# Kernel optimization log

Measured on AMD Instinct MI355X. Metric: run time of the kernel, lower is better.

## Reference

```python
import jax, jax.numpy as jnp
import numpy as np

T, B, D_IN, H = 512, 128, 1024, 2048

def _lstm_cell(x, h, c, W_ih, W_hh, b):
    # PyTorch LSTMCell gate order: i, f, g, o
    gates = x @ W_ih.T + h @ W_hh.T + b  # [B, 4H]
    i, f, g, o = jnp.split(gates, 4, axis=-1)
    c_new = jax.nn.sigmoid(f) * c + jax.nn.sigmoid(i) * jnp.tanh(g)
    h_new = jax.nn.sigmoid(o) * jnp.tanh(c_new)
    return h_new, c_new

def setup_inputs() -> dict:
    key = jax.random.key(0)
    ks = jax.random.split(key, 12)
    k = 1.0 / np.sqrt(H)  # torch LSTMCell init range
    u = lambda kk, shape: jax.random.uniform(kk, shape, jnp.float32, -k, k)
    return {
        "input_seq": jax.random.normal(ks[0], (T, B, D_IN), jnp.float32),
        "h0": jax.random.normal(ks[1], (2, B, H), jnp.float32),
        "c0": jax.random.normal(ks[2], (2, B, H), jnp.float32),
        "W_ih0": u(ks[3], (4 * H, D_IN)),
        "W_hh0": u(ks[4], (4 * H, H)),
        "b0": u(ks[5], (4 * H,)),
        "W_ih1": u(ks[6], (4 * H, H)),
        "W_hh1": u(ks[7], (4 * H, H)),
        "b1": u(ks[8], (4 * H,)),
    }

def reference(input_seq, h0, c0, W_ih0, W_hh0, b0, W_ih1, W_hh1, b1):
    def step(carry, x_t):
        h0_, c0_, h1_, c1_ = carry
        h0n, c0n = _lstm_cell(x_t, h0_, c0_, W_ih0, W_hh0, b0)
        h1n, c1n = _lstm_cell(h0n, h1_, c1_, W_ih1, W_hh1, b1)
        return (h0n, c0n, h1n, c1n), None

    init = (h0[0], c0[0], h0[1], c0[1])
    (h0f, c0f, h1f, c1f), _ = jax.lax.scan(step, init, input_seq)
    return h1f  # last layer hidden at final timestep [B, H]
```

## Files before the change

### kernel.cpp

```cpp
#include <hip/hip_runtime.h>
#include <stdint.h>
#include <stddef.h>

#define T_STEPS 512
#define B_SZ    128
#define DIN     1024
#define H_SZ    2048
#define NG      8192
#define BH      (B_SZ * H_SZ)

typedef __attribute__((ext_vector_type(8))) short bf16x8;
typedef __attribute__((ext_vector_type(4))) float f32x4;

static __device__ __forceinline__ unsigned short f2bf(float x) {
  unsigned int u = __float_as_uint(x);
  u += 0x7fffu + ((u >> 16) & 1u);
  return (unsigned short)(u >> 16);
}

static __device__ __forceinline__ float sigm(float x) {
  return 1.0f / (1.0f + __expf(-x));
}
static __device__ __forceinline__ float tanh_(float x) {
  float e = __expf(-2.0f * fabsf(x));
  float t = (1.0f - e) / (1.0f + e);
  return x < 0.0f ? -t : t;
}

static __device__ __forceinline__ void async_load16(const void* gsrc, void* ldst) {
  __builtin_amdgcn_global_load_lds(
      (__attribute__((address_space(1))) void*)(const_cast<void*>(gsrc)),
      (__attribute__((address_space(3))) void*)ldst,
      16, 0, 0);
}

static __device__ __forceinline__ void wg_barrier_pinned() {
  __builtin_amdgcn_s_barrier();
  asm volatile("" ::: "memory");
  __builtin_amdgcn_sched_barrier(0);
}

__global__ void cvt_x_bf16(const float4* __restrict__ in, ushort4* __restrict__ out, int n4) {
  int i = blockIdx.x * blockDim.x + threadIdx.x;
  int st = gridDim.x * blockDim.x;
  for (; i < n4; i += st) {
    float4 v = in[i];
    ushort4 o;
    o.x = f2bf(v.x); o.y = f2bf(v.y); o.z = f2bf(v.z); o.w = f2bf(v.w);
    out[i] = o;
  }
}

__global__ void build_wcat(const float* __restrict__ wa, const float* __restrict__ wb,
                           unsigned short* __restrict__ outw, int ka, int K) {
  int k = blockIdx.x * blockDim.x + threadIdx.x;
  int n = blockIdx.y;
  if (k >= K) return;
  int kb = K - ka;
  float v = (k < ka) ? wa[(size_t)n * ka + k]
                     : wb[(size_t)n * kb + (k - ka)];
  outw[(size_t)n * K + k] = f2bf(v);
}

__global__ void init_state(const float* __restrict__ h0, const float* __restrict__ c0,
                           unsigned short* __restrict__ hb0, unsigned short* __restrict__ hb1,
                           float* __restrict__ cws) {
  int i = blockIdx.x * blockDim.x + threadIdx.x;
  if (i < BH) {
    hb0[i] = f2bf(h0[i]);
    hb1[i] = f2bf(h0[BH + i]);
    cws[i] = c0[i];
    cws[BH + i] = c0[BH + i];
  }
}

template<int K, int KSPLIT>
static __device__ __forceinline__ void lstm_step_body(
    unsigned short (*Bbuf)[128 * 64],
    const unsigned short* __restrict__ a0,
    const unsigned short* __restrict__ a1,
    const unsigned short* __restrict__ w,
    const float* __restrict__ bias,
    float* __restrict__ c,
    unsigned short* __restrict__ hout,
    float* __restrict__ fout,
    int tid, int lane, int wv, int n0h)
{
  constexpr int KT = K >> 6;
  f32x4 acc[8] = {};

  const int arow = wv * 16 + (lane & 15);
  const unsigned short* r0p = a0 + (size_t)arow * KSPLIT;
  const unsigned short* r1p = a1 + (size_t)arow * H_SZ;
  const int klo = (lane >> 4) << 3;

  auto loadA = [&](int kt, bf16x8 (&A)[2]) {
    const int kb = kt << 6;
    const bool sA = kb < KSPLIT;
    const unsigned short* bp = (sA ? r0p : r1p) + (sA ? kb : kb - KSPLIT) + klo;
    A[0] = *(const bf16x8*)(bp);
    A[1] = *(const bf16x8*)(bp + 32);
  };

  auto stageB = [&](int kt) {
    const int kb = kt << 6;
#pragma unroll
    for (int it = 0; it < 2; ++it) {
      int cid = it * 512 + tid;
      int nl  = cid >> 3;
      int chs = (cid & 7) ^ (nl & 7);
      int nn  = ((nl >> 5) << 11) + n0h + (nl & 31);
      const unsigned short* src = w + (size_t)nn * K + kb + (chs << 3);
      async_load16(src, &Bbuf[kt & 3][(it * 512 + wv * 64) * 8]);
    }
  };

  auto iter = [&](int kt, bf16x8 (&A)[2]) {
    if (kt + 3 < KT) stageB(kt + 3);
    const int bq = kt & 3;
#pragma unroll
    for (int kkk = 0; kkk < 2; ++kkk) {
      const int ch = kkk * 4 + (lane >> 4);
      const int cswz = (ch ^ (lane & 7)) << 3;
      bf16x8 bfr[8];
#pragma unroll
      for (int ct = 0; ct < 8; ++ct)
        bfr[ct] = *(const bf16x8*)&Bbuf[bq][(ct * 16 + (lane & 15)) * 64 + cswz];
#pragma unroll
      for (int ct = 0; ct < 8; ++ct)
        acc[ct] = __builtin_amdgcn_mfma_f32_16x16x32_bf16(A[kkk], bfr[ct], acc[ct], 0, 0, 0);
    }
    if (kt + 4 < KT) loadA(kt + 4, A);
    int rem = KT - 1 - kt;
    if (rem >= 4)      asm volatile("s_waitcnt vmcnt(10)" ::: "memory");
    else if (rem == 3) asm volatile("s_waitcnt vmcnt(8)"  ::: "memory");
    else if (rem == 2) asm volatile("s_waitcnt vmcnt(4)"  ::: "memory");
    else if (rem == 1) asm volatile("s_waitcnt vmcnt(0)"  ::: "memory");
    wg_barrier_pinned();
  };

  asm volatile("s_waitcnt vmcnt(0)" ::: "memory");

  bf16x8 A0[2], A1[2], A2[2], A3[2];
  stageB(0); loadA(0, A0);
  stageB(1); loadA(1, A1);
  stageB(2); loadA(2, A2);
  loadA(3, A3);
  asm volatile("s_waitcnt vmcnt(12)" ::: "memory");
  wg_barrier_pinned();

  for (int kt = 0; kt < KT; kt += 4) {
    iter(kt,     A0);
    iter(kt + 1, A1);
    iter(kt + 2, A2);
    iter(kt + 3, A3);
  }

#pragma unroll
  for (int p = 0; p < 2; ++p) {
    const int hc = n0h + p * 16 + (lane & 15);
    const float bi  = bias[hc];
    const float bff = bias[H_SZ + hc];
    const float bg  = bias[2 * H_SZ + hc];
    const float bo  = bias[3 * H_SZ + hc];
#pragma unroll
    for (int r = 0; r < 4; ++r) {
      int row = wv * 16 + ((lane >> 4) << 2) + r;
      size_t idx = (size_t)row * H_SZ + hc;
      float iv = sigm(acc[p    ][r] + bi);
      float fv = sigm(acc[p + 2][r] + bff);
      float gv = tanh_(acc[p + 4][r] + bg);
      float ov = sigm(acc[p + 6][r] + bo);
      float cn = fv * c[idx] + iv * gv;
      c[idx] = cn;
      float hn = ov * tanh_(cn);
      hout[idx] = f2bf(hn);
      if (fout) fout[idx] = hn;
    }
  }
}

template<int K, int KSPLIT>
__global__ __launch_bounds__(512, 2) void lstm_one(
    const unsigned short* __restrict__ a0, const unsigned short* __restrict__ a1,
    const unsigned short* __restrict__ w,  const float* __restrict__ bias,
    float* __restrict__ c, unsigned short* __restrict__ hout, float* __restrict__ fout)
{
  __shared__ __align__(16) unsigned short Bbuf[4][128 * 64];
  const int tid = threadIdx.x, lane = tid & 63, wv = tid >> 6;
  const int n0h = blockIdx.x << 5;
  lstm_step_body<K, KSPLIT>(Bbuf, a0, a1, w, bias, c, hout, fout, tid, lane, wv, n0h);
}

template<int K1, int KS1, int K2, int KS2>
__global__ __launch_bounds__(512, 2) void lstm_pair(
    const unsigned short* __restrict__ a0_1, const unsigned short* __restrict__ a1_1,
    const unsigned short* __restrict__ w1,   const float* __restrict__ bias1,
    float* __restrict__ c1, unsigned short* __restrict__ h1out,
    const unsigned short* __restrict__ a0_2, const unsigned short* __restrict__ a1_2,
    const unsigned short* __restrict__ w2,   const float* __restrict__ bias2,
    float* __restrict__ c2, unsigned short* __restrict__ h2out)
{
  __shared__ __align__(16) unsigned short Bbuf[4][128 * 64];
  const int tid = threadIdx.x, lane = tid & 63, wv = tid >> 6;
  if (blockIdx.x < 64) {
    const int n0h = blockIdx.x << 5;
    lstm_step_body<K1, KS1>(Bbuf, a0_1, a1_1, w1, bias1, c1, h1out, nullptr, tid, lane, wv, n0h);
  } else {
    const int n0h = (blockIdx.x - 64) << 5;
    lstm_step_body<K2, KS2>(Bbuf, a0_2, a1_2, w2, bias2, c2, h2out, nullptr, tid, lane, wv, n0h);
  }
}

extern "C" void kernel_launch(void* const* d_in, const int* in_sizes, int n_in,
                              void* d_out, int out_size, void* d_ws, size_t ws_size,
                              hipStream_t stream) {
  (void)in_sizes; (void)n_in; (void)out_size; (void)ws_size;
  const float* x    = (const float*)d_in[0];
  const float* h0   = (const float*)d_in[1];
  const float* c0   = (const float*)d_in[2];
  const float* Wih0 = (const float*)d_in[3];
  const float* Whh0 = (const float*)d_in[4];
  const float* b0   = (const float*)d_in[5];
  const float* Wih1 = (const float*)d_in[6];
  const float* Whh1 = (const float*)d_in[7];
  const float* b1   = (const float*)d_in[8];
  float* out = (float*)d_out;

  unsigned short* xbf = (unsigned short*)d_ws;
  unsigned short* Wc0 = xbf + (size_t)T_STEPS * B_SZ * DIN;
  unsigned short* Wc1 = Wc0 + (size_t)NG * 3072;
  unsigned short* hb0 = Wc1 + (size_t)NG * 4096;
  unsigned short* hb1 = hb0 + 2 * (size_t)BH;
  float*          cws = (float*)(hb1 + 2 * (size_t)BH);

  cvt_x_bf16<<<dim3(4096), dim3(256), 0, stream>>>(
      (const float4*)x, (ushort4*)xbf, T_STEPS * B_SZ * DIN / 4);
  build_wcat<<<dim3(12, NG), dim3(256), 0, stream>>>(Wih0, Whh0, Wc0, DIN, 3072);
  build_wcat<<<dim3(16, NG), dim3(256), 0, stream>>>(Wih1, Whh1, Wc1, H_SZ, 4096);
  init_state<<<dim3(BH / 256), dim3(256), 0, stream>>>(h0, c0, hb0, hb1, cws);

  lstm_one<3072, 1024><<<dim3(64), dim3(512), 0, stream>>>(
      xbf, hb0 + 0, Wc0, b0, cws, hb0 + BH, nullptr);

  for (int t = 0; t < T_STEPS - 1; ++t) {
    const unsigned short* h0cur = hb0 + (size_t)((t + 1) & 1) * BH;
    lstm_pair<4096, 2048, 3072, 1024><<<dim3(128), dim3(512), 0, stream>>>(
           h0cur, hb1 + (size_t)(t & 1) * BH, Wc1, b1,
                    cws + BH, hb1 + (size_t)((t + 1) & 1) * BH,
         xbf + (size_t)(t + 1) * B_SZ * DIN, h0cur, Wc0, b0,
                    cws, hb0 + (size_t)(t & 1) * BH);
  }
  lstm_one<4096, 2048><<<dim3(64), dim3(512), 0, stream>>>(
      hb0 + 0, hb1 + BH, Wc1, b1, cws + BH, hb1 + 0, out);
}
```

Measured before the change: 23.29 ms.

## Switch LSTM step GEMM to 32x32x16 MFMA with 4-wave workgroups

Replaces the 16x16x32 bf16 MFMA tiling with 32x32x16 tiles. Each wave now covers 32 batch rows and all 128 gate columns using four 16-wide accumulators. Workgroups shrink from 512 to 256 threads (4 waves), so each thread stages four LDS chunks per k-tile, and the vmcnt thresholds and epilogue row mapping are updated to match. The larger MFMA shape reduces LDS B-fragment reads per FLOP, and the barrier after the last k-tile is skipped. The cost is fewer waves per workgroup for hiding latency and more accumulator registers per thread.

Measured after the change: 26.35 ms. 13.1% more time.

```diff
diff --git a/kernel.cpp b/kernel.cpp
--- a/kernel.cpp
+++ b/kernel.cpp
@@ -10,7 +10,7 @@
 #define BH      (B_SZ * H_SZ)
 
 typedef __attribute__((ext_vector_type(8))) short bf16x8;
-typedef __attribute__((ext_vector_type(4))) float f32x4;
+typedef __attribute__((ext_vector_type(16))) float f32x16;
 
 static __device__ __forceinline__ unsigned short f2bf(float x) {
   unsigned int u = __float_as_uint(x);
@@ -87,66 +87,66 @@
     int tid, int lane, int wv, int n0h)
 {
   constexpr int KT = K >> 6;
-  f32x4 acc[8] = {};
-
-  const int arow = wv * 16 + (lane & 15);
+  f32x16 acc[4] = {};
+
+  const int arow = wv * 32 + (lane & 31);
   const unsigned short* r0p = a0 + (size_t)arow * KSPLIT;
   const unsigned short* r1p = a1 + (size_t)arow * H_SZ;
-  const int klo = (lane >> 4) << 3;
-
-  auto loadA = [&](int kt, bf16x8 (&A)[2]) {
+  const int khi = (lane >> 5) << 3;
+
+  auto loadA = [&](int kt, bf16x8 (&A)[4]) {
     const int kb = kt << 6;
     const bool sA = kb < KSPLIT;
-    const unsigned short* bp = (sA ? r0p : r1p) + (sA ? kb : kb - KSPLIT) + klo;
-    A[0] = *(const bf16x8*)(bp);
-    A[1] = *(const bf16x8*)(bp + 32);
+    const unsigned short* bp = (sA ? r0p : r1p) + (sA ? kb : kb - KSPLIT) + khi;
+#pragma unroll
+    for (int cc = 0; cc < 4; ++cc)
+      A[cc] = *(const bf16x8*)(bp + cc * 16);
   };
 
   auto stageB = [&](int kt) {
     const int kb = kt << 6;
 #pragma unroll
-    for (int it = 0; it < 2; ++it) {
-      int cid = it * 512 + tid;
+    for (int it = 0; it < 4; ++it) {
+      int cid = it * 256 + tid;
       int nl  = cid >> 3;
       int chs = (cid & 7) ^ (nl & 7);
       int nn  = ((nl >> 5) << 11) + n0h + (nl & 31);
       const unsigned short* src = w + (size_t)nn * K + kb + (chs << 3);
-      async_load16(src, &Bbuf[kt & 3][(it * 512 + wv * 64) * 8]);
+      async_load16(src, &Bbuf[kt & 3][(it * 256 + wv * 64) * 8]);
     }
   };
 
-  auto iter = [&](int kt, bf16x8 (&A)[2]) {
+  auto iter = [&](int kt, bf16x8 (&A)[4]) {
     if (kt + 3 < KT) stageB(kt + 3);
     const int bq = kt & 3;
 #pragma unroll
-    for (int kkk = 0; kkk < 2; ++kkk) {
-      const int ch = kkk * 4 + (lane >> 4);
-      const int cswz = (ch ^ (lane & 7)) << 3;
-      bf16x8 bfr[8];
-#pragma unroll
-      for (int ct = 0; ct < 8; ++ct)
-        bfr[ct] = *(const bf16x8*)&Bbuf[bq][(ct * 16 + (lane & 15)) * 64 + cswz];
-#pragma unroll
-      for (int ct = 0; ct < 8; ++ct)
-        acc[ct] = __builtin_amdgcn_mfma_f32_16x16x32_bf16(A[kkk], bfr[ct], acc[ct], 0, 0, 0);
+    for (int cc = 0; cc < 4; ++cc) {
+      const int chunk = (((cc << 1) + (lane >> 5)) ^ (lane & 7)) << 3;
+      bf16x8 bfr[4];
+#pragma unroll
+      for (int ct = 0; ct < 4; ++ct)
+        bfr[ct] = *(const bf16x8*)&Bbuf[bq][(ct * 32 + (lane & 31)) * 64 + chunk];
+#pragma unroll
+      for (int ct = 0; ct < 4; ++ct)
+        acc[ct] = __builtin_amdgcn_mfma_f32_32x32x16_bf16(A[cc], bfr[ct], acc[ct], 0, 0, 0);
     }
     if (kt + 4 < KT) loadA(kt + 4, A);
     int rem = KT - 1 - kt;
-    if (rem >= 4)      asm volatile("s_waitcnt vmcnt(10)" ::: "memory");
-    else if (rem == 3) asm volatile("s_waitcnt vmcnt(8)"  ::: "memory");
-    else if (rem == 2) asm volatile("s_waitcnt vmcnt(4)"  ::: "memory");
+    if (rem >= 4)      asm volatile("s_waitcnt vmcnt(20)" ::: "memory");
+    else if (rem == 3) asm volatile("s_waitcnt vmcnt(16)" ::: "memory");
+    else if (rem == 2) asm volatile("s_waitcnt vmcnt(8)"  ::: "memory");
     else if (rem == 1) asm volatile("s_waitcnt vmcnt(0)"  ::: "memory");
-    wg_barrier_pinned();
+    if (rem > 0) wg_barrier_pinned();
   };
 
   asm volatile("s_waitcnt vmcnt(0)" ::: "memory");
 
-  bf16x8 A0[2], A1[2], A2[2], A3[2];
+  bf16x8 A0[4], A1[4], A2[4], A3[4];
   stageB(0); loadA(0, A0);
   stageB(1); loadA(1, A1);
   stageB(2); loadA(2, A2);
   loadA(3, A3);
-  asm volatile("s_waitcnt vmcnt(12)" ::: "memory");
+  asm volatile("s_waitcnt vmcnt(24)" ::: "memory");
   wg_barrier_pinned();
 
   for (int kt = 0; kt < KT; kt += 4) {
@@ -156,32 +156,31 @@
     iter(kt + 3, A3);
   }
 
-#pragma unroll
-  for (int p = 0; p < 2; ++p) {
-    const int hc = n0h + p * 16 + (lane & 15);
-    const float bi  = bias[hc];
-    const float bff = bias[H_SZ + hc];
-    const float bg  = bias[2 * H_SZ + hc];
-    const float bo  = bias[3 * H_SZ + hc];
-#pragma unroll
-    for (int r = 0; r < 4; ++r) {
-      int row = wv * 16 + ((lane >> 4) << 2) + r;
-      size_t idx = (size_t)row * H_SZ + hc;
-      float iv = sigm(acc[p    ][r] + bi);
-      float fv = sigm(acc[p + 2][r] + bff);
-      float gv = tanh_(acc[p + 4][r] + bg);
-      float ov = sigm(acc[p + 6][r] + bo);
-      float cn = fv * c[idx] + iv * gv;
-      c[idx] = cn;
-      float hn = ov * tanh_(cn);
-      hout[idx] = f2bf(hn);
-      if (fout) fout[idx] = hn;
-    }
+  const int hc = n0h + (lane & 31);
+  const float bi  = bias[hc];
+  const float bff = bias[H_SZ + hc];
+  const float bg  = bias[2 * H_SZ + hc];
+  const float bo  = bias[3 * H_SZ + hc];
+  const int rbase = wv * 32 + ((lane >> 5) << 2);
+
+#pragma unroll
+  for (int reg = 0; reg < 16; ++reg) {
+    int row = rbase + (reg & 3) + ((reg >> 2) << 3);
+    size_t idx = (size_t)row * H_SZ + hc;
+    float iv = sigm(acc[0][reg] + bi);
+    float fv = sigm(acc[1][reg] + bff);
+    float gv = tanh_(acc[2][reg] + bg);
+    float ov = sigm(acc[3][reg] + bo);
+    float cn = fv * c[idx] + iv * gv;
+    c[idx] = cn;
+    float hn = ov * tanh_(cn);
+    hout[idx] = f2bf(hn);
+    if (fout) fout[idx] = hn;
   }
 }
 
 template<int K, int KSPLIT>
-__global__ __launch_bounds__(512, 2) void lstm_one(
+__global__ __launch_bounds__(256) void lstm_one(
     const unsigned short* __restrict__ a0, const unsigned short* __restrict__ a1,
     const unsigned short* __restrict__ w,  const float* __restrict__ bias,
     float* __restrict__ c, unsigned short* __restrict__ hout, float* __restrict__ fout)
@@ -193,7 +192,7 @@
 }
 
 template<int K1, int KS1, int K2, int KS2>
-__global__ __launch_bounds__(512, 2) void lstm_pair(
+__global__ __launch_bounds__(256) void lstm_pair(
     const unsigned short* __restrict__ a0_1, const unsigned short* __restrict__ a1_1,
     const unsigned short* __restrict__ w1,   const float* __restrict__ bias1,
     float* __restrict__ c1, unsigned short* __restrict__ h1out,
@@ -240,17 +239,17 @@
   build_wcat<<<dim3(16, NG), dim3(256), 0, stream>>>(Wih1, Whh1, Wc1, H_SZ, 4096);
   init_state<<<dim3(BH / 256), dim3(256), 0, stream>>>(h0, c0, hb0, hb1, cws);
 
-  lstm_one<3072, 1024><<<dim3(64), dim3(512), 0, stream>>>(
+  lstm_one<3072, 1024><<<dim3(64), dim3(256), 0, stream>>>(
       xbf, hb0 + 0, Wc0, b0, cws, hb0 + BH, nullptr);
 
   for (int t = 0; t < T_STEPS - 1; ++t) {
     const unsigned short* h0cur = hb0 + (size_t)((t + 1) & 1) * BH;
-    lstm_pair<4096, 2048, 3072, 1024><<<dim3(128), dim3(512), 0, stream>>>(
+    lstm_pair<4096, 2048, 3072, 1024><<<dim3(128), dim3(256), 0, stream>>>(
            h0cur, hb1 + (size_t)(t & 1) * BH, Wc1, b1,
                     cws + BH, hb1 + (size_t)((t + 1) & 1) * BH,
          xbf + (size_t)(t + 1) * B_SZ * DIN, h0cur, Wc0, b0,
                     cws, hb0 + (size_t)(t & 1) * BH);
   }
-  lstm_one<4096, 2048><<<dim3(64), dim3(512), 0, stream>>>(
+  lstm_one<4096, 2048><<<dim3(64), dim3(256), 0, stream>>>(
       hb0 + 0, hb1 + BH, Wc1, b1, cws + BH, hb1 + 0, out);
 }
```
